# Optimization experiments

Hardware: AMD Instinct MI355X
Metric: run time of the kernel (lower is better)

The kernel has to match this reference:

```python
import jax, jax.numpy as jnp
import numpy as np

# SPU(x) = x^2 - 0.5 for x >= 0, sigmoid(-x) - 1 for x < 0 (networks.SPU)

def _spu(x):
    return jnp.where(x >= 0, x * x - 0.5, jax.nn.sigmoid(-x) - 1.0)


def _spu_grad(x):
    xc = jnp.clip(x, -50.0, 50.0)  # avoid cosh overflow; masked out anyway
    neg_grad = -0.5 / (jnp.cosh(xc) + 1.0)
    return jnp.where(x >= 0, 2.0 * x, jnp.where(x <= -50.0, 0.0, neg_grad))


def setup_inputs() -> dict:
    key = jax.random.key(0)
    k1, k2 = jax.random.split(key)
    bs, n = 64, 65536
    l = 3.0 * jax.random.normal(k1, (bs, n), dtype=jnp.float32)
    u = l + jax.random.uniform(k2, (bs, n), dtype=jnp.float32, minval=0.0, maxval=4.0)
    return {"l": l, "u": u}


def reference(l, u):
    # --- spu(l, u): per-element sound linear bounds lw*x+lb <= SPU(x) <= uw*x+ub ---
    sl = _spu(l)
    su = _spu(u)

    # chord between (l, spu(l)) and (u, spu(u))  [calc_line_between]
    a_lu = (su - sl) / (u - l + 1e-8)
    b_lu = sl - l * a_lu

    # tangent at midpoint  [spu_tangent_parametrised, t=0.5]
    mid = 0.5 * (l + u)
    a_t = _spu_grad(mid)
    b_t = _spu(mid) - a_t * mid

    neg = u < 0
    pos = (~neg) & (l > 0)
    mixed = (~neg) & (~pos)
    normal = mixed & (su > sl)   # spu_mixed_normal_u
    # small = mixed & ~normal   -> spu_mixed_small_u

    # mixed lower-bound candidates
    # c0: y = -0.5
    # c1: chord from l to 0: spu(0) = -0.5
    a1 = (-0.5 - sl) / (-l + 1e-8)
    b1 = sl - l * a1
    # c2: tangent at u/2 (midpoint of [0, u]) -- only for the normal_u case
    h = 0.5 * u
    a2 = _spu_grad(h)
    b2 = _spu(h) - a2 * h

    def area(a, b):
        # find_area_proxy: -(u-l)*(a*l+b + a*u+b)
        return -(u - l) * (a * (l + u) + 2.0 * b)

    ar0 = area(0.0, -0.5)
    ar1 = area(a1, b1)
    ar2 = jnp.where(normal, area(a2, b2), jnp.inf)  # small_u has only 2 candidates
    idx = jnp.argmin(jnp.stack([ar0, ar1, ar2], axis=0), axis=0)
    a_m = jnp.where(idx == 0, 0.0, jnp.where(idx == 1, a1, a2))
    b_m = jnp.where(idx == 0, -0.5, jnp.where(idx == 1, b1, b2))

    lw = jnp.where(neg, a_lu, jnp.where(pos, a_t, a_m))
    lb = jnp.where(neg, b_lu, jnp.where(pos, b_t, b_m))
    uw = jnp.where(neg, a_t, jnp.where(pos | normal, a_lu, 0.0))
    ub = jnp.where(neg, b_t, jnp.where(pos | normal, b_lu, sl))

    # --- backsubstitution into the input layer (prev.al = l, prev.au = u) ---
    # nal is diagonal (lw) + bias column (lb); substitute() with constant input
    # bounds reduces to selecting l for positive coeffs, u for non-positive.
    nl = lb + jnp.where(lw > 0, lw * l, lw * u)
    nu = ub + jnp.where(uw > 0, uw * u, uw * l)
    return nl, nu
```

## Files before the change

kernel.cpp:

```cpp
#include <hip/hip_runtime.h>
#include <math.h>

typedef float f32x4 __attribute__((ext_vector_type(4)));

__device__ __forceinline__ float frcp(float x) { return __builtin_amdgcn_rcpf(x); }

__device__ __forceinline__ void spu_bounds(float l, float u, float& nl, float& nu) {
    const float mid = 0.5f * (l + u);
    const float dlu = u - l;

    const float e_l = __expf(l);
    const float e_u = __expf(u);
    const float e_m = __expf(mid);
    const float r_l = frcp(1.0f + e_l);
    const float r_u = frcp(1.0f + e_u);
    const float r_m = frcp(1.0f + e_m);
    const float rl0 = frcp(1e-8f - l);

    const bool mpos = (mid >= 0.0f);
    const float sl = (l >= 0.0f) ? fmaf(l, l, -0.5f) : (r_l - 1.0f);
    const float su = (u >= 0.0f) ? fmaf(u, u, -0.5f) : (r_u - 1.0f);
    const float sm = mpos ? fmaf(mid, mid, -0.5f) : (r_m - 1.0f);
    const float gmh = mpos ? (-mid) : (0.5f * e_m * r_m * r_m);

    const float TL = fmaf(gmh, dlu, sm);

    const bool neg    = (u < 0.0f);
    const bool pos    = (!neg) && (l > 0.0f);
    const bool normal = (!neg) && (!pos) && (su > sl);

    const float a1 = (-0.5f - sl) * rl0;
    const float n1 = fmaf(a1, dlu, sl);
    const float p  = fmaf(0.25f * u, u, 0.5f);
    const float n2 = fmaf(u, l, -p);

    const float x1 = n1 + sl;
    const float x2 = fmaf(u, fmaf(0.5f, u, l), -1.0f);

    const bool  c1   = (x1 > -1.0f);
    const float nl01 = c1 ? n1 : -0.5f;
    const float xb   = c1 ? x1 : -1.0f;
    const bool  c2   = normal && (x2 > xb);
    const float nlm  = c2 ? n2 : nl01;

    nl = neg ? su : (pos ? TL : nlm);
    nu = neg ? TL : ((pos || normal) ? su : sl);
}

__device__ __forceinline__ void spu_bounds4(const f32x4 lv, const f32x4 uv,
                                            f32x4& a, f32x4& b) {
    float a0, b0, a1, b1, a2, b2, a3, b3;
    spu_bounds(lv.x, uv.x, a0, b0);
    spu_bounds(lv.y, uv.y, a1, b1);
    spu_bounds(lv.z, uv.z, a2, b2);
    spu_bounds(lv.w, uv.w, a3, b3);
    a.x = a0; a.y = a1; a.z = a2; a.w = a3;
    b.x = b0; b.y = b1; b.z = b2; b.w = b3;
}

__global__ void __launch_bounds__(256) spu_pointwise_kernel(
        const float* __restrict__ l, const float* __restrict__ u,
        float* __restrict__ out_nl, float* __restrict__ out_nu,
        int n4, int n) {
    const int tid = blockIdx.x * blockDim.x + threadIdx.x;
    const int stride = gridDim.x * blockDim.x;
    const int pairs = n4 >> 1;

    const f32x4* __restrict__ l4 = reinterpret_cast<const f32x4*>(l);
    const f32x4* __restrict__ u4 = reinterpret_cast<const f32x4*>(u);
    f32x4* __restrict__ nl4 = reinterpret_cast<f32x4*>(out_nl);
    f32x4* __restrict__ nu4 = reinterpret_cast<f32x4*>(out_nu);

    for (int i = tid; i < pairs; i += stride) {
        const int j = i + pairs;
        const f32x4 lv0 = l4[i];
        const f32x4 uv0 = u4[i];
        const f32x4 lv1 = l4[j];
        const f32x4 uv1 = u4[j];
        f32x4 a0, b0, a1, b1;
        spu_bounds4(lv0, uv0, a0, b0);
        spu_bounds4(lv1, uv1, a1, b1);
        __builtin_nontemporal_store(a0, nl4 + i);
        __builtin_nontemporal_store(b0, nu4 + i);
        __builtin_nontemporal_store(a1, nl4 + j);
        __builtin_nontemporal_store(b1, nu4 + j);
    }

    for (int i = 2 * pairs + tid; i < n4; i += stride) {
        const f32x4 lv = l4[i];
        const f32x4 uv = u4[i];
        f32x4 a, b;
        spu_bounds4(lv, uv, a, b);
        __builtin_nontemporal_store(a, nl4 + i);
        __builtin_nontemporal_store(b, nu4 + i);
    }

    for (int i = n4 * 4 + tid; i < n; i += stride) {
        spu_bounds(l[i], u[i], out_nl[i], out_nu[i]);
    }
}

extern "C" void kernel_launch(void* const* d_in, const int* in_sizes, int n_in,
                              void* d_out, int out_size, void* d_ws, size_t ws_size,
                              hipStream_t stream) {
    const float* l = (const float*)d_in[0];
    const float* u = (const float*)d_in[1];
    float* out = (float*)d_out;

    const int n = in_sizes[0];
    float* out_nl = out;
    float* out_nu = out + n;

    const int n4 = n / 4;
    const int pairs = n4 / 2;
    const int block = 256;
    int grid = (pairs + block - 1) / block;
    if (grid > 8192) grid = 8192;
    if (grid < 1) grid = 1;

    spu_pointwise_kernel<<<grid, block, 0, stream>>>(l, u, out_nl, out_nu, n4, n);
}
```

Before: 14.39 us.

## Software-prefetch next iteration's inputs and halve grid size

```diff
diff --git a/kernel.cpp b/kernel.cpp
--- a/kernel.cpp
+++ b/kernel.cpp
@@ -64,39 +64,48 @@
         int n4, int n) {
     const int tid = blockIdx.x * blockDim.x + threadIdx.x;
     const int stride = gridDim.x * blockDim.x;
-    const int pairs = n4 >> 1;
+    const int half = n4 >> 1;
 
     const f32x4* __restrict__ l4 = reinterpret_cast<const f32x4*>(l);
     const f32x4* __restrict__ u4 = reinterpret_cast<const f32x4*>(u);
     f32x4* __restrict__ nl4 = reinterpret_cast<f32x4*>(out_nl);
     f32x4* __restrict__ nu4 = reinterpret_cast<f32x4*>(out_nu);
 
-    for (int i = tid; i < pairs; i += stride) {
-        const int j = i + pairs;
-        const f32x4 lv0 = l4[i];
-        const f32x4 uv0 = u4[i];
-        const f32x4 lv1 = l4[j];
-        const f32x4 uv1 = u4[j];
+    int i = tid;
+    f32x4 lv0, uv0, lv1, uv1;
+    if (i < half) {
+        lv0 = l4[i];        uv0 = u4[i];
+        lv1 = l4[i + half]; uv1 = u4[i + half];
+    }
+    while (i < half) {
+        const int inext = i + stride;
+        f32x4 plv0, puv0, plv1, puv1;
+        if (inext < half) {
+            plv0 = l4[inext];        puv0 = u4[inext];
+            plv1 = l4[inext + half]; puv1 = u4[inext + half];
+        }
         f32x4 a0, b0, a1, b1;
         spu_bounds4(lv0, uv0, a0, b0);
         spu_bounds4(lv1, uv1, a1, b1);
         __builtin_nontemporal_store(a0, nl4 + i);
         __builtin_nontemporal_store(b0, nu4 + i);
-        __builtin_nontemporal_store(a1, nl4 + j);
-        __builtin_nontemporal_store(b1, nu4 + j);
+        __builtin_nontemporal_store(a1, nl4 + i + half);
+        __builtin_nontemporal_store(b1, nu4 + i + half);
+        lv0 = plv0; uv0 = puv0; lv1 = plv1; uv1 = puv1;
+        i = inext;
     }
 
-    for (int i = 2 * pairs + tid; i < n4; i += stride) {
-        const f32x4 lv = l4[i];
-        const f32x4 uv = u4[i];
+    for (int k = 2 * half + tid; k < n4; k += stride) {
+        const f32x4 lv = l4[k];
+        const f32x4 uv = u4[k];
         f32x4 a, b;
         spu_bounds4(lv, uv, a, b);
-        __builtin_nontemporal_store(a, nl4 + i);
-        __builtin_nontemporal_store(b, nu4 + i);
+        __builtin_nontemporal_store(a, nl4 + k);
+        __builtin_nontemporal_store(b, nu4 + k);
     }
 
-    for (int i = n4 * 4 + tid; i < n; i += stride) {
-        spu_bounds(l[i], u[i], out_nl[i], out_nu[i]);
+    for (int k = n4 * 4 + tid; k < n; k += stride) {
+        spu_bounds(l[k], u[k], out_nl[k], out_nu[k]);
     }
 }
 
@@ -112,9 +121,9 @@
     float* out_nu = out + n;
 
     const int n4 = n / 4;
-    const int pairs = n4 / 2;
+    const int half = n4 / 2;
     const int block = 256;
-    int grid = (pairs + block - 1) / block;
+    int grid = (half + block - 1) / block / 2;
     if (grid > 8192) grid = 8192;
     if (grid < 1) grid = 1;
 
```

New measurement: 16.90 us. 17.4% more time.
